# Kernel optimization log

Measured on AMD Instinct MI355X. Metric: run time of the kernel, lower is better.

## Reference

```python
import jax, jax.numpy as jnp
import numpy as np

ALPHA = 32.0
RANK = 16


def setup_inputs() -> dict:
    key = jax.random.key(0)
    ks = jax.random.split(key, 6)
    d_in, d_out, r = 4096, 4096, RANK
    x = jax.random.normal(ks[0], (4, 2048, d_in), dtype=jnp.float32)
    W = jax.random.normal(ks[1], (d_out, d_in), dtype=jnp.float32) * (1.0 / np.sqrt(d_in))
    bias = jax.random.normal(ks[2], (d_out,), dtype=jnp.float32) * 0.02
    B_lora = jax.random.normal(ks[3], (d_out, r), dtype=jnp.float32) * (1.0 / np.sqrt(r))
    A_lora = jax.random.normal(ks[4], (r, d_in), dtype=jnp.float32) * (1.0 / np.sqrt(d_in))
    delta_bias = jax.random.normal(ks[5], (d_out,), dtype=jnp.float32) * 0.02
    return {"x": x, "W": W, "bias": bias, "B_lora": B_lora, "A_lora": A_lora, "delta_bias": delta_bias}


def reference(x, W, bias, B_lora, A_lora, delta_bias):
    # LoRALinear.forward with adapter_enabled=True:
    # y = x @ (W + (alpha/rank) * B @ A).T + bias + (alpha/rank) * delta_bias
    # Expressed as base GEMM + two small low-rank GEMMs (same math, no
    # [out, in] delta-weight materialization).
    scale = ALPHA / RANK
    base = jnp.einsum('bsi,oi->bso', x, W)              # [B,S,out]
    xa = jnp.einsum('bsi,ri->bsr', x, A_lora)           # [B,S,r]
    delta = jnp.einsum('bsr,or->bso', xa, B_lora)       # [B,S,out]
    return base + scale * delta + bias + scale * delta_bias
```

## Files before the change

kernel.cpp:

```cpp
#include <hip/hip_runtime.h>
#include <stdint.h>

#define M_DIM 8192
#define N_DIM 4096
#define K_DIM 4096

typedef __attribute__((ext_vector_type(4))) float f32x4;
typedef __attribute__((ext_vector_type(8))) __bf16 bf16x8;

__device__ __forceinline__ unsigned short f2bf(float f) {
  unsigned int u = __builtin_bit_cast(unsigned int, f);
  u += 0x7FFFu + ((u >> 16) & 1u);
  return (unsigned short)(u >> 16);
}

__device__ __forceinline__ void load16_lds(const void* g, void* l) {
  __builtin_amdgcn_global_load_lds(
      (__attribute__((address_space(1))) void*)g,
      (__attribute__((address_space(3))) void*)l,
      16, 0, 0);
}

#define WAITVM(N) asm volatile("s_waitcnt vmcnt(" #N ")" ::: "memory")
#define BARRIER() asm volatile("s_barrier" ::: "memory")

__global__ __launch_bounds__(256) void cvt_x_kernel(const float* __restrict__ x,
                                                    unsigned short* __restrict__ xb) {
  const int n8 = (M_DIM * K_DIM) / 8;
  int i = blockIdx.x * blockDim.x + threadIdx.x;
  const int stride = gridDim.x * blockDim.x;
  for (; i < n8; i += stride) {
    const float4* p = (const float4*)x + (size_t)i * 2;
    const float4 a = p[0];
    const float4 b = p[1];
    uint4 o;
    o.x = (unsigned)f2bf(a.x) | ((unsigned)f2bf(a.y) << 16);
    o.y = (unsigned)f2bf(a.z) | ((unsigned)f2bf(a.w) << 16);
    o.z = (unsigned)f2bf(b.x) | ((unsigned)f2bf(b.y) << 16);
    o.w = (unsigned)f2bf(b.z) | ((unsigned)f2bf(b.w) << 16);
    ((uint4*)xb)[i] = o;
  }
}

__global__ __launch_bounds__(256) void build_wb_kernel(const float* __restrict__ W,
                                                       const float* __restrict__ B_lora,
                                                       const float* __restrict__ A_lora,
                                                       unsigned short* __restrict__ wb) {
  __shared__ float As[64][17];
  __shared__ float Bs[64][17];
  const int t = threadIdx.x;
  const int i0 = blockIdx.x * 64;
  const int o0 = blockIdx.y * 64;
  {
    const int c = t & 63;
    #pragma unroll
    for (int rr = (t >> 6); rr < 16; rr += 4)
      As[c][rr] = A_lora[rr * K_DIM + i0 + c];
    const int r2 = t & 15;
    #pragma unroll
    for (int oo = (t >> 4); oo < 64; oo += 16)
      Bs[oo][r2] = B_lora[(o0 + oo) * 16 + r2];
  }
  __syncthreads();
  const int ci = t & 63;
  const int og = t >> 6;
  float areg[16];
  #pragma unroll
  for (int r = 0; r < 16; ++r) areg[r] = As[ci][r];
  const int i = i0 + ci;
  #pragma unroll 4
  for (int j = 0; j < 16; ++j) {
    const int ol = og * 16 + j;
    float d = 0.f;
    #pragma unroll
    for (int r = 0; r < 16; ++r) d += Bs[ol][r] * areg[r];
    const size_t idx = (size_t)(o0 + ol) * K_DIM + i;
    wb[idx] = f2bf(W[idx] + 2.0f * d);
  }
}

__global__ __launch_bounds__(512, 2) void gemm_kernel(const unsigned short* __restrict__ xb,
                                                      const unsigned short* __restrict__ wb,
                                                      const float* __restrict__ bias,
                                                      const float* __restrict__ dbias,
                                                      float* __restrict__ out) {
  constexpr int BK = 64;
  constexpr int NT = K_DIM / BK;
  __shared__ char As[65536];
  __shared__ char Bs[65536];

  const int t = threadIdx.x;
  const int w = t >> 6, l = t & 63;
  const int wr = w >> 2, wc = w & 3;
  constexpr int NBN = N_DIM / 256;
  constexpr int NWG = (M_DIM / 256) * NBN;
  int bid = (int)blockIdx.x;
  bid = (bid & 7) * (NWG >> 3) + (bid >> 3);
  const int m0 = (bid / NBN) * 256;
  const int n0 = (bid % NBN) * 256;

  const int trow = t >> 3;
  const int scol = ((t & 7) ^ (trow & 7)) * 8;
  const int rowoffA[4] = {0, 128, 64, 192};
  const int ldsoffA[4] = {0, 16384, 8192, 24576};
  const unsigned short* gAp[4];
  #pragma unroll
  for (int j = 0; j < 4; ++j)
    gAp[j] = xb + (size_t)(m0 + rowoffA[j] + trow) * K_DIM + scol;
  const unsigned short* gBp[4];
  #pragma unroll
  for (int j = 0; j < 4; ++j) {
    const int rp = j * 64 + trow;
    const int gr = (rp & 31) + ((rp >> 5) & 3) * 64 + (rp >> 7) * 32;
    gBp[j] = wb + (size_t)(n0 + gr) * K_DIM + scol;
  }
  const int wlds = w * 1024;

  const int swz = (l & 7) << 4;
  const int rdk = (l >> 4) * 16;
  const int rdA = (wr * 128 + (l & 15)) * 128;
  const int rdB = (wc * 32 + (l & 15)) * 128;

  f32x4 acc[8][4];
  #pragma unroll
  for (int i = 0; i < 8; ++i)
    #pragma unroll
    for (int j = 0; j < 4; ++j) acc[i][j] = f32x4{0.f, 0.f, 0.f, 0.f};
  bf16x8 af[4][2], bf[4][2];

#define STAGE_A(CUR, SLOT, KT) \
  load16_lds(gAp[SLOT] + (KT), As + (CUR) * 32768 + ldsoffA[SLOT] + wlds)
#define STAGE_B(CUR, SLOT, KT) \
  load16_lds(gBp[SLOT] + (KT), Bs + (CUR) * 32768 + (SLOT) * 8192 + wlds)

#define READ_AH(CUR, MH)                                                      \
  {                                                                           \
    const char* base_ = As + (CUR) * 32768 + rdA + (MH) * 8192;               \
    _Pragma("unroll") for (int mf_ = 0; mf_ < 4; ++mf_)                       \
      _Pragma("unroll") for (int ks_ = 0; ks_ < 2; ++ks_)                     \
        af[mf_][ks_] = *(const bf16x8*)(base_ + mf_ * 2048 +                  \
                                        ((ks_ * 64 + rdk) ^ swz));            \
  }
#define READ_BH(CUR, NH)                                                      \
  {                                                                           \
    const char* base_ = Bs + (CUR) * 32768 + rdB + (NH) * 16384;              \
    _Pragma("unroll") for (int nf_ = 0; nf_ < 2; ++nf_)                       \
      _Pragma("unroll") for (int ks_ = 0; ks_ < 2; ++ks_)                     \
        bf[(NH) * 2 + nf_][ks_] = *(const bf16x8*)(base_ + nf_ * 2048 +       \
                                                   ((ks_ * 64 + rdk) ^ swz)); \
  }
#define QUAD(MH, NH)                                                          \
  {                                                                           \
    __builtin_amdgcn_s_setprio(1);                                            \
    _Pragma("unroll") for (int mf_ = 0; mf_ < 4; ++mf_)                       \
      _Pragma("unroll") for (int nf_ = 0; nf_ < 2; ++nf_)                     \
        _Pragma("unroll") for (int ks_ = 0; ks_ < 2; ++ks_)                   \
          acc[(MH) * 4 + mf_][(NH) * 2 + nf_] =                               \
              __builtin_amdgcn_mfma_f32_16x16x32_bf16(                        \
                  af[mf_][ks_], bf[(NH) * 2 + nf_][ks_],                      \
                  acc[(MH) * 4 + mf_][(NH) * 2 + nf_], 0, 0, 0);              \
    __builtin_amdgcn_s_setprio(0);                                            \
  }

  STAGE_A(0, 0, 0); STAGE_A(0, 1, 0);
  STAGE_B(0, 0, 0); STAGE_B(0, 1, 0);
  STAGE_B(0, 2, 0); STAGE_B(0, 3, 0);
  STAGE_A(0, 2, 0); STAGE_A(0, 3, 0);
  WAITVM(4);
  BARRIER();

  int cur = 0;
  for (int kt = 0; kt < NT - 1; ++kt) {
    const int kn = (kt + 1) * BK;
    const int nxt = cur ^ 1;
    READ_AH(cur, 0); READ_BH(cur, 0);
    STAGE_A(nxt, 0, kn); STAGE_A(nxt, 1, kn);
    BARRIER(); QUAD(0, 0); WAITVM(4); BARRIER();
    READ_BH(cur, 1);
    STAGE_B(nxt, 0, kn); STAGE_B(nxt, 1, kn);
    BARRIER(); QUAD(0, 1); WAITVM(4); BARRIER();
    READ_AH(cur, 1);
    STAGE_B(nxt, 2, kn); STAGE_B(nxt, 3, kn);
    BARRIER(); QUAD(1, 1); BARRIER();
    STAGE_A(nxt, 2, kn); STAGE_A(nxt, 3, kn);
    BARRIER(); QUAD(1, 0); WAITVM(4); BARRIER();
    cur = nxt;
  }
  READ_AH(cur, 0); READ_BH(cur, 0);
  BARRIER(); QUAD(0, 0); WAITVM(2); BARRIER();
  READ_BH(cur, 1);
  BARRIER(); QUAD(0, 1); WAITVM(0); BARRIER();
  READ_AH(cur, 1);
  QUAD(1, 1); QUAD(1, 0);

  float bv[4];
  #pragma unroll
  for (int nf = 0; nf < 4; ++nf) {
    const int c = n0 + wc * 64 + nf * 16 + (l & 15);
    bv[nf] = bias[c] + 2.0f * dbias[c];
  }
  #pragma unroll
  for (int mf = 0; mf < 8; ++mf) {
    const int r0 = m0 + wr * 128 + mf * 16 + ((l >> 4) << 2);
    #pragma unroll
    for (int nf = 0; nf < 4; ++nf) {
      const int c = n0 + wc * 64 + nf * 16 + (l & 15);
      const f32x4 v = acc[mf][nf];
      #pragma unroll
      for (int j = 0; j < 4; ++j)
        out[(size_t)(r0 + j) * N_DIM + c] = v[j] + bv[nf];
    }
  }
#undef STAGE_A
#undef STAGE_B
#undef READ_AH
#undef READ_BH
#undef QUAD
}

__global__ __launch_bounds__(256) void xa_kernel(const float* __restrict__ x,
                                                 const float* __restrict__ A_lora,
                                                 float* __restrict__ xa) {
  const int m = blockIdx.x;
  const int t = threadIdx.x;
  float acc[16];
  #pragma unroll
  for (int r = 0; r < 16; ++r) acc[r] = 0.f;
  const float* xr = x + (size_t)m * K_DIM;
  for (int k = t; k < K_DIM; k += 256) {
    const float xv = xr[k];
    #pragma unroll
    for (int r = 0; r < 16; ++r) acc[r] += xv * A_lora[r * K_DIM + k];
  }
  __shared__ float red[16][4];
  #pragma unroll
  for (int r = 0; r < 16; ++r) {
    float v = acc[r];
    for (int off = 32; off > 0; off >>= 1) v += __shfl_down(v, off, 64);
    if ((t & 63) == 0) red[r][t >> 6] = v;
  }
  __syncthreads();
  if (t < 16) xa[(size_t)m * 16 + t] = red[t][0] + red[t][1] + red[t][2] + red[t][3];
}

__global__ __launch_bounds__(256) void fgemm_kernel(const float* __restrict__ x,
                                                    const float* __restrict__ W,
                                                    const float* __restrict__ bias,
                                                    const float* __restrict__ B_lora,
                                                    const float* __restrict__ dbias,
                                                    const float* __restrict__ xa,
                                                    float* __restrict__ out) {
  __shared__ float As[64][17];
  __shared__ float Ws[64][17];
  const int t = threadIdx.x;
  const int m0 = (blockIdx.x >> 6) * 64;
  const int n0 = (blockIdx.x & 63) * 64;
  const int tx = t & 15, ty = t >> 4;
  float c[4][4] = {};
  for (int kt = 0; kt < K_DIM; kt += 16) {
    #pragma unroll
    for (int e = 0; e < 4; ++e) {
      const int q = t + e * 256;
      const int r = q >> 4, k = q & 15;
      As[r][k] = x[(size_t)(m0 + r) * K_DIM + kt + k];
      Ws[r][k] = W[(size_t)(n0 + r) * K_DIM + kt + k];
    }
    __syncthreads();
    #pragma unroll
    for (int k = 0; k < 16; ++k) {
      float a[4], b[4];
      #pragma unroll
      for (int ii = 0; ii < 4; ++ii) a[ii] = As[ty * 4 + ii][k];
      #pragma unroll
      for (int jj = 0; jj < 4; ++jj) b[jj] = Ws[tx * 4 + jj][k];
      #pragma unroll
      for (int ii = 0; ii < 4; ++ii)
        #pragma unroll
        for (int jj = 0; jj < 4; ++jj) c[ii][jj] += a[ii] * b[jj];
    }
    __syncthreads();
  }
  #pragma unroll
  for (int ii = 0; ii < 4; ++ii) {
    const int row = m0 + ty * 4 + ii;
    #pragma unroll
    for (int jj = 0; jj < 4; ++jj) {
      const int col = n0 + tx * 4 + jj;
      float d = 0.f;
      #pragma unroll
      for (int r = 0; r < 16; ++r) d += xa[(size_t)row * 16 + r] * B_lora[col * 16 + r];
      out[(size_t)row * N_DIM + col] = c[ii][jj] + 2.0f * d + bias[col] + 2.0f * dbias[col];
    }
  }
}

extern "C" void kernel_launch(void* const* d_in, const int* in_sizes, int n_in,
                              void* d_out, int out_size, void* d_ws, size_t ws_size,
                              hipStream_t stream) {
  const float* x = (const float*)d_in[0];
  const float* W = (const float*)d_in[1];
  const float* bias = (const float*)d_in[2];
  const float* B_lora = (const float*)d_in[3];
  const float* A_lora = (const float*)d_in[4];
  const float* dbias = (const float*)d_in[5];
  float* out = (float*)d_out;

  const size_t NEED = (size_t)M_DIM * K_DIM * 2 + (size_t)N_DIM * K_DIM * 2;
  if (ws_size >= NEED) {
    unsigned short* xb = (unsigned short*)d_ws;
    unsigned short* wb = xb + (size_t)M_DIM * K_DIM;
    cvt_x_kernel<<<2048, 256, 0, stream>>>(x, xb);
    build_wb_kernel<<<dim3(64, 64), 256, 0, stream>>>(W, B_lora, A_lora, wb);
    gemm_kernel<<<(M_DIM / 256) * (N_DIM / 256), 512, 0, stream>>>(xb, wb, bias, dbias, out);
  } else {
    float* xa = (float*)d_ws;
    xa_kernel<<<M_DIM, 256, 0, stream>>>(x, A_lora, xa);
    fgemm_kernel<<<(M_DIM / 64) * (N_DIM / 64), 256, 0, stream>>>(x, W, bias, B_lora, dbias, xa, out);
  }
}
```

Before: 557.9 us.

## Double-buffer LDS fragment registers to prefetch next tile during MFMA quads

Splits the A and B fragment registers into two sets and reorders the main loop so the next k-tile's first A/B fragments are read from LDS while the current tile's last MFMA quads execute. The waitcnt and barrier placement is adjusted to match. The aim is to hide LDS read latency behind MFMA work, in exchange for more VGPR pressure and a more fragile sync schedule that could race.

Measured after the change: 545.1 us. 2.3% less time.

```diff
diff --git a/kernel.cpp b/kernel.cpp
--- a/kernel.cpp
+++ b/kernel.cpp
@@ -126,30 +126,31 @@
   for (int i = 0; i < 8; ++i)
     #pragma unroll
     for (int j = 0; j < 4; ++j) acc[i][j] = f32x4{0.f, 0.f, 0.f, 0.f};
-  bf16x8 af[4][2], bf[4][2];
+  bf16x8 afA[4][2], afB[4][2];
+  bf16x8 bfA[2][2], bfB[2][2];
 
 #define STAGE_A(CUR, SLOT, KT) \
   load16_lds(gAp[SLOT] + (KT), As + (CUR) * 32768 + ldsoffA[SLOT] + wlds)
 #define STAGE_B(CUR, SLOT, KT) \
   load16_lds(gBp[SLOT] + (KT), Bs + (CUR) * 32768 + (SLOT) * 8192 + wlds)
 
-#define READ_AH(CUR, MH)                                                      \
+#define READ_A(CUR, MH, DST)                                                  \
   {                                                                           \
     const char* base_ = As + (CUR) * 32768 + rdA + (MH) * 8192;               \
     _Pragma("unroll") for (int mf_ = 0; mf_ < 4; ++mf_)                       \
       _Pragma("unroll") for (int ks_ = 0; ks_ < 2; ++ks_)                     \
-        af[mf_][ks_] = *(const bf16x8*)(base_ + mf_ * 2048 +                  \
-                                        ((ks_ * 64 + rdk) ^ swz));            \
-  }
-#define READ_BH(CUR, NH)                                                      \
+        DST[mf_][ks_] = *(const bf16x8*)(base_ + mf_ * 2048 +                 \
+                                         ((ks_ * 64 + rdk) ^ swz));           \
+  }
+#define READ_B(CUR, NH, DST)                                                  \
   {                                                                           \
     const char* base_ = Bs + (CUR) * 32768 + rdB + (NH) * 16384;              \
     _Pragma("unroll") for (int nf_ = 0; nf_ < 2; ++nf_)                       \
       _Pragma("unroll") for (int ks_ = 0; ks_ < 2; ++ks_)                     \
-        bf[(NH) * 2 + nf_][ks_] = *(const bf16x8*)(base_ + nf_ * 2048 +       \
-                                                   ((ks_ * 64 + rdk) ^ swz)); \
-  }
-#define QUAD(MH, NH)                                                          \
+        DST[nf_][ks_] = *(const bf16x8*)(base_ + nf_ * 2048 +                 \
+                                         ((ks_ * 64 + rdk) ^ swz));           \
+  }
+#define QUAD(MH, NH, AFR, BFR)                                                \
   {                                                                           \
     __builtin_amdgcn_s_setprio(1);                                            \
     _Pragma("unroll") for (int mf_ = 0; mf_ < 4; ++mf_)                       \
@@ -157,7 +158,7 @@
         _Pragma("unroll") for (int ks_ = 0; ks_ < 2; ++ks_)                   \
           acc[(MH) * 4 + mf_][(NH) * 2 + nf_] =                               \
               __builtin_amdgcn_mfma_f32_16x16x32_bf16(                        \
-                  af[mf_][ks_], bf[(NH) * 2 + nf_][ks_],                      \
+                  AFR[mf_][ks_], BFR[nf_][ks_],                               \
                   acc[(MH) * 4 + mf_][(NH) * 2 + nf_], 0, 0, 0);              \
     __builtin_amdgcn_s_setprio(0);                                            \
   }
@@ -166,32 +167,36 @@
   STAGE_B(0, 0, 0); STAGE_B(0, 1, 0);
   STAGE_B(0, 2, 0); STAGE_B(0, 3, 0);
   STAGE_A(0, 2, 0); STAGE_A(0, 3, 0);
-  WAITVM(4);
+  WAITVM(2);
   BARRIER();
+  READ_A(0, 0, afA); READ_B(0, 0, bfA);
 
   int cur = 0;
   for (int kt = 0; kt < NT - 1; ++kt) {
     const int kn = (kt + 1) * BK;
     const int nxt = cur ^ 1;
-    READ_AH(cur, 0); READ_BH(cur, 0);
+    READ_B(cur, 1, bfB);
     STAGE_A(nxt, 0, kn); STAGE_A(nxt, 1, kn);
-    BARRIER(); QUAD(0, 0); WAITVM(4); BARRIER();
-    READ_BH(cur, 1);
+    BARRIER(); QUAD(0, 0, afA, bfA); WAITVM(2); BARRIER();
+    READ_A(cur, 1, afB);
     STAGE_B(nxt, 0, kn); STAGE_B(nxt, 1, kn);
-    BARRIER(); QUAD(0, 1); WAITVM(4); BARRIER();
-    READ_AH(cur, 1);
     STAGE_B(nxt, 2, kn); STAGE_B(nxt, 3, kn);
-    BARRIER(); QUAD(1, 1); BARRIER();
+    BARRIER(); QUAD(0, 1, afA, bfB); WAITVM(4); BARRIER();
+    QUAD(1, 1, afB, bfB);
+    READ_A(nxt, 0, afA);
+    WAITVM(2); BARRIER();
     STAGE_A(nxt, 2, kn); STAGE_A(nxt, 3, kn);
-    BARRIER(); QUAD(1, 0); WAITVM(4); BARRIER();
+    BARRIER(); QUAD(1, 0, afB, bfA);
+    READ_B(nxt, 0, bfA);
+    WAITVM(2); BARRIER();
     cur = nxt;
   }
-  READ_AH(cur, 0); READ_BH(cur, 0);
-  BARRIER(); QUAD(0, 0); WAITVM(2); BARRIER();
-  READ_BH(cur, 1);
-  BARRIER(); QUAD(0, 1); WAITVM(0); BARRIER();
-  READ_AH(cur, 1);
-  QUAD(1, 1); QUAD(1, 0);
+  READ_B(cur, 1, bfB);
+  BARRIER(); QUAD(0, 0, afA, bfA); WAITVM(0); BARRIER();
+  READ_A(cur, 1, afB);
+  QUAD(0, 1, afA, bfB);
+  QUAD(1, 1, afB, bfB);
+  QUAD(1, 0, afB, bfA);
 
   float bv[4];
   #pragma unroll
@@ -213,8 +218,8 @@
   }
 #undef STAGE_A
 #undef STAGE_B
-#undef READ_AH
-#undef READ_BH
+#undef READ_A
+#undef READ_B
 #undef QUAD
 }
 
```
